# Performance work log

Hardware: AMD Instinct MI355X
Metric: run time of the kernel (lower is better)

The kernel has to match this reference:

```python
import jax, jax.numpy as jnp
import numpy as np

D = 64  # max disparity search range (d in the torch module)


def setup_inputs() -> dict:
    key = jax.random.key(0)
    k1, k2 = jax.random.split(key)
    B, C, H, W = 8, 128, 128, 256
    x1 = jax.random.normal(k1, (B, C, H, W), dtype=jnp.float32)
    x2 = jax.random.normal(k2, (B, C, H, W), dtype=jnp.float32)
    return {"x1": x1, "x2": x2}


def _corr_volume(x1, x2, d):
    # result[n, i, h, w] = (1/C) * sum_c x1[n,c,h,w] * x2[n,c,h,w-i], zero where w-i < 0
    n, c, h, w = x2.shape
    slices = []
    for i in range(d + 1):
        # shift x2 right by i columns, zero-padding on the left
        shifted = jnp.pad(x2[:, :, :, : w - i] if i > 0 else x2,
                          ((0, 0), (0, 0), (0, 0), (i, 0)))
        slices.append(jnp.sum(x1 * shifted, axis=1))  # [n, h, w]
    cv = jnp.stack(slices, axis=1)  # [n, d+1, h, w]
    return cv * (1.0 / c)


def reference(x1, x2):
    return _corr_volume(x1, x2, D)
```

## Files before the change

### kernel.cpp

```cpp
#include <hip/hip_runtime.h>
#include <hip/hip_fp16.h>


constexpr int B   = 8;
constexpr int C   = 128;
constexpr int H   = 128;
constexpr int W   = 256;
constexpr int NI  = 65;
constexpr int HW  = H * W;
constexpr int CHW = C * HW;
constexpr int KC2 = 16;
constexpr int X2W = 320;

typedef _Float16 half2v __attribute__((ext_vector_type(2)));

__device__ inline unsigned int pack2(float a, float b) {
    __half2 h = __floats2half2_rn(a, b);
    return __builtin_bit_cast(unsigned int, h);
}

__device__ inline float fdot2f(unsigned int a, unsigned int b, float c) {
#if __has_builtin(__builtin_amdgcn_fdot2)
    return __builtin_amdgcn_fdot2(__builtin_bit_cast(half2v, a),
                                  __builtin_bit_cast(half2v, b), c, false);
#else
    __half2 ha = __builtin_bit_cast(__half2, a);
    __half2 hb = __builtin_bit_cast(__half2, b);
    float2 fa = __half22float2(ha), fb = __half22float2(hb);
    return fmaf(fa.x, fb.x, fmaf(fa.y, fb.y, c));
#endif
}

__global__ __launch_bounds__(512, 4)
void corr_volume_kernel(const float* __restrict__ x1,
                        const float* __restrict__ x2,
                        float* __restrict__ out) {
    const int h   = blockIdx.x;
    const int n   = blockIdx.y;
    const int tid = threadIdx.x;
    const int l   = tid & 63;
    const int q   = tid >> 6;

    __shared__ unsigned int x1h[KC2][W];
    __shared__ unsigned int x2h[KC2][X2W];

    float acc[8][4];
    #pragma unroll
    for (int il = 0; il < 8; ++il)
        #pragma unroll
        for (int wl = 0; wl < 4; ++wl) acc[il][wl] = 0.0f;
    float acc64[4] = {0.f, 0.f, 0.f, 0.f};

    const int j0 = 4 * l - 8 * q + 56;

    const float* x1g = x1 + n * CHW + h * W;
    const float* x2g = x2 + n * CHW + h * W;

    if (tid < 256) {
        const int r  = tid >> 4;
        const int cq = tid & 15;
        *(uint4*)&x2h[r][4 * cq] = make_uint4(0u, 0u, 0u, 0u);
    }

    for (int c0 = 0; c0 < C; c0 += 2 * KC2) {
        #pragma unroll
        for (int k = 0; k < 2; ++k) {
            const int e  = tid + k * 512;
            const int r  = e >> 6;
            const int cq = e & 63;
            {
                const float4 lo = *(const float4*)(x1g + (c0 + 2 * r) * HW + 4 * cq);
                const float4 hi = *(const float4*)(x1g + (c0 + 2 * r + 1) * HW + 4 * cq);
                uint4 p;
                p.x = pack2(lo.x, hi.x); p.y = pack2(lo.y, hi.y);
                p.z = pack2(lo.z, hi.z); p.w = pack2(lo.w, hi.w);
                *(uint4*)&x1h[r][4 * cq] = p;
            }
            {
                const float4 lo = *(const float4*)(x2g + (c0 + 2 * r) * HW + 4 * cq);
                const float4 hi = *(const float4*)(x2g + (c0 + 2 * r + 1) * HW + 4 * cq);
                uint4 p;
                p.x = pack2(lo.x, hi.x); p.y = pack2(lo.y, hi.y);
                p.z = pack2(lo.z, hi.z); p.w = pack2(lo.w, hi.w);
                *(uint4*)&x2h[r][64 + 4 * cq] = p;
            }
        }
        __syncthreads();

        #pragma unroll 2
        for (int c2 = 0; c2 < KC2; ++c2) {
            const uint4 a4 = *(const uint4*)&x1h[c2][4 * l];
            const unsigned int aw[4] = {a4.x, a4.y, a4.z, a4.w};
            const uint4 b0 = *(const uint4*)&x2h[c2][j0];
            const uint4 b1 = *(const uint4*)&x2h[c2][j0 + 4];
            const uint4 b2 = *(const uint4*)&x2h[c2][j0 + 8];
            const unsigned int bw[12] = {b0.x, b0.y, b0.z, b0.w,
                                         b1.x, b1.y, b1.z, b1.w,
                                         b2.x, b2.y, b2.z, b2.w};
            #pragma unroll
            for (int il = 0; il < 8; ++il)
                #pragma unroll
                for (int wl = 0; wl < 4; ++wl)
                    acc[il][wl] = fdot2f(aw[wl], bw[wl - il + 8], acc[il][wl]);

            if (q == 0) {
                const uint4 d = *(const uint4*)&x2h[c2][4 * l];
                const unsigned int dw[4] = {d.x, d.y, d.z, d.w};
                #pragma unroll
                for (int wl = 0; wl < 4; ++wl)
                    acc64[wl] = fdot2f(aw[wl], dw[wl], acc64[wl]);
            }
        }
        __syncthreads();
    }

    const float scale = 1.0f / (float)C;
    float* outg = out + n * (NI * HW) + h * W + 4 * l;
    #pragma unroll
    for (int il = 0; il < 8; ++il) {
        const int i = 8 * q + il;
        *(float4*)(outg + i * HW) =
            make_float4(acc[il][0] * scale, acc[il][1] * scale,
                        acc[il][2] * scale, acc[il][3] * scale);
    }
    if (q == 0) {
        *(float4*)(outg + 64 * HW) =
            make_float4(acc64[0] * scale, acc64[1] * scale,
                        acc64[2] * scale, acc64[3] * scale);
    }
}

extern "C" void kernel_launch(void* const* d_in, const int* in_sizes, int n_in,
                              void* d_out, int out_size, void* d_ws, size_t ws_size,
                              hipStream_t stream) {
    const float* x1 = (const float*)d_in[0];
    const float* x2 = (const float*)d_in[1];
    float* out = (float*)d_out;
    dim3 grid(H, B);
    corr_volume_kernel<<<grid, 512, 0, stream>>>(x1, x2, out);
}
```

Baseline: 320.0 us.

## Double-buffer shared memory and prefetch next channel chunk into registers

Splits the x1/x2 shared tiles into two buffers. The next chunk's global loads are issued into registers before computing on the current buffer, then packed and stored into the other buffer afterwards, which removes one barrier per iteration. The aim is to hide global load latency behind the fdot2 compute. In exchange it doubles LDS use to about 72KB per block and holds 32 extra VGPRs for the prefetched float4s, which may lower occupancy under launch_bounds(512,4).

```diff
diff --git a/kernel.cpp b/kernel.cpp
--- a/kernel.cpp
+++ b/kernel.cpp
@@ -11,6 +11,7 @@
 constexpr int CHW = C * HW;
 constexpr int KC2 = 16;
 constexpr int X2W = 320;
+constexpr int NCHUNK = C / (2 * KC2);
 
 typedef _Float16 half2v __attribute__((ext_vector_type(2)));
 
@@ -41,8 +42,8 @@
     const int l   = tid & 63;
     const int q   = tid >> 6;
 
-    __shared__ unsigned int x1h[KC2][W];
-    __shared__ unsigned int x2h[KC2][X2W];
+    __shared__ unsigned int x1h[2][KC2][W];
+    __shared__ unsigned int x2h[2][KC2][X2W];
 
     float acc[8][4];
     #pragma unroll
@@ -56,44 +57,66 @@
     const float* x1g = x1 + n * CHW + h * W;
     const float* x2g = x2 + n * CHW + h * W;
 
-    if (tid < 256) {
-        const int r  = tid >> 4;
-        const int cq = tid & 15;
-        *(uint4*)&x2h[r][4 * cq] = make_uint4(0u, 0u, 0u, 0u);
+    {
+        const int bufi = tid >> 8;
+        const int r    = (tid >> 4) & 15;
+        const int cq   = tid & 15;
+        *(uint4*)&x2h[bufi][r][4 * cq] = make_uint4(0u, 0u, 0u, 0u);
     }
 
-    for (int c0 = 0; c0 < C; c0 += 2 * KC2) {
+    const int sr = tid >> 6;
+    const int sc = (tid & 63) * 4;
+
+    float4 L[8];
+
+    auto issue = [&](int c0) {
         #pragma unroll
-        for (int k = 0; k < 2; ++k) {
-            const int e  = tid + k * 512;
-            const int r  = e >> 6;
-            const int cq = e & 63;
-            {
-                const float4 lo = *(const float4*)(x1g + (c0 + 2 * r) * HW + 4 * cq);
-                const float4 hi = *(const float4*)(x1g + (c0 + 2 * r + 1) * HW + 4 * cq);
-                uint4 p;
-                p.x = pack2(lo.x, hi.x); p.y = pack2(lo.y, hi.y);
-                p.z = pack2(lo.z, hi.z); p.w = pack2(lo.w, hi.w);
-                *(uint4*)&x1h[r][4 * cq] = p;
-            }
-            {
-                const float4 lo = *(const float4*)(x2g + (c0 + 2 * r) * HW + 4 * cq);
-                const float4 hi = *(const float4*)(x2g + (c0 + 2 * r + 1) * HW + 4 * cq);
-                uint4 p;
-                p.x = pack2(lo.x, hi.x); p.y = pack2(lo.y, hi.y);
-                p.z = pack2(lo.z, hi.z); p.w = pack2(lo.w, hi.w);
-                *(uint4*)&x2h[r][64 + 4 * cq] = p;
-            }
+        for (int hh = 0; hh < 2; ++hh) {
+            const int r = sr + 8 * hh;
+            const float* a = x1g + (c0 + 2 * r) * HW + sc;
+            const float* b = x2g + (c0 + 2 * r) * HW + sc;
+            L[4 * hh + 0] = *(const float4*)(a);
+            L[4 * hh + 1] = *(const float4*)(a + HW);
+            L[4 * hh + 2] = *(const float4*)(b);
+            L[4 * hh + 3] = *(const float4*)(b + HW);
         }
-        __syncthreads();
+    };
+    auto commit = [&](int bufi) {
+        #pragma unroll
+        for (int hh = 0; hh < 2; ++hh) {
+            const int r = sr + 8 * hh;
+            uint4 p;
+            p.x = pack2(L[4 * hh + 0].x, L[4 * hh + 1].x);
+            p.y = pack2(L[4 * hh + 0].y, L[4 * hh + 1].y);
+            p.z = pack2(L[4 * hh + 0].z, L[4 * hh + 1].z);
+            p.w = pack2(L[4 * hh + 0].w, L[4 * hh + 1].w);
+            *(uint4*)&x1h[bufi][r][sc] = p;
+            uint4 s;
+            s.x = pack2(L[4 * hh + 2].x, L[4 * hh + 3].x);
+            s.y = pack2(L[4 * hh + 2].y, L[4 * hh + 3].y);
+            s.z = pack2(L[4 * hh + 2].z, L[4 * hh + 3].z);
+            s.w = pack2(L[4 * hh + 2].w, L[4 * hh + 3].w);
+            *(uint4*)&x2h[bufi][r][64 + sc] = s;
+        }
+    };
+
+    issue(0);
+    commit(0);
+    __syncthreads();
+
+    #pragma unroll
+    for (int t = 0; t < NCHUNK; ++t) {
+        const int cur = t & 1;
+
+        if (t + 1 < NCHUNK) issue((t + 1) * 2 * KC2);
 
         #pragma unroll 2
         for (int c2 = 0; c2 < KC2; ++c2) {
-            const uint4 a4 = *(const uint4*)&x1h[c2][4 * l];
+            const uint4 a4 = *(const uint4*)&x1h[cur][c2][4 * l];
             const unsigned int aw[4] = {a4.x, a4.y, a4.z, a4.w};
-            const uint4 b0 = *(const uint4*)&x2h[c2][j0];
-            const uint4 b1 = *(const uint4*)&x2h[c2][j0 + 4];
-            const uint4 b2 = *(const uint4*)&x2h[c2][j0 + 8];
+            const uint4 b0 = *(const uint4*)&x2h[cur][c2][j0];
+            const uint4 b1 = *(const uint4*)&x2h[cur][c2][j0 + 4];
+            const uint4 b2 = *(const uint4*)&x2h[cur][c2][j0 + 8];
             const unsigned int bw[12] = {b0.x, b0.y, b0.z, b0.w,
                                          b1.x, b1.y, b1.z, b1.w,
                                          b2.x, b2.y, b2.z, b2.w};
@@ -104,14 +127,18 @@
                     acc[il][wl] = fdot2f(aw[wl], bw[wl - il + 8], acc[il][wl]);
 
             if (q == 0) {
-                const uint4 d = *(const uint4*)&x2h[c2][4 * l];
+                const uint4 d = *(const uint4*)&x2h[cur][c2][4 * l];
                 const unsigned int dw[4] = {d.x, d.y, d.z, d.w};
                 #pragma unroll
                 for (int wl = 0; wl < 4; ++wl)
                     acc64[wl] = fdot2f(aw[wl], dw[wl], acc64[wl]);
             }
         }
-        __syncthreads();
+
+        if (t + 1 < NCHUNK) {
+            commit((t + 1) & 1);
+            __syncthreads();
+        }
     }
 
     const float scale = 1.0f / (float)C;
```

Result: no change. 314.3 us (-1.8%).

## Process two rows per block with 16 disparities per thread

Applied to the files above, without the earlier changes.

Each block now handles two image rows, with four waves per row, and each thread accumulates 16 disparities instead of 8. This raises register reuse of the loaded x2 window, since 20 words are loaded for 64 dot products, and halves the grid. The channel chunk is halved, the trailing barrier is dropped in favour of a leading one, and the disparity-64 term reuses already-loaded registers. The cost is higher register pressure from 64+ accumulators and fewer blocks, which may reduce occupancy.

```diff
diff --git a/kernel.cpp b/kernel.cpp
--- a/kernel.cpp
+++ b/kernel.cpp
@@ -9,8 +9,9 @@
 constexpr int NI  = 65;
 constexpr int HW  = H * W;
 constexpr int CHW = C * HW;
-constexpr int KC2 = 16;
+constexpr int KC2 = 8;
 constexpr int X2W = 320;
+constexpr int NCHUNK = C / (2 * KC2);
 
 typedef _Float16 half2v __attribute__((ext_vector_type(2)));
 
@@ -35,95 +36,100 @@
 void corr_volume_kernel(const float* __restrict__ x1,
                         const float* __restrict__ x2,
                         float* __restrict__ out) {
-    const int h   = blockIdx.x;
+    const int bh  = blockIdx.x;
     const int n   = blockIdx.y;
     const int tid = threadIdx.x;
     const int l   = tid & 63;
     const int q   = tid >> 6;
+    const int hsel = q >> 2;
+    const int qi   = q & 3;
 
-    __shared__ unsigned int x1h[KC2][W];
-    __shared__ unsigned int x2h[KC2][X2W];
+    __shared__ unsigned int x1h[2][KC2][W];
+    __shared__ unsigned int x2h[2][KC2][X2W];
 
-    float acc[8][4];
+    float acc[16][4];
     #pragma unroll
-    for (int il = 0; il < 8; ++il)
+    for (int il = 0; il < 16; ++il)
         #pragma unroll
         for (int wl = 0; wl < 4; ++wl) acc[il][wl] = 0.0f;
     float acc64[4] = {0.f, 0.f, 0.f, 0.f};
 
-    const int j0 = 4 * l - 8 * q + 56;
+    const int j0a = 4 * l - 16 * qi + 48;
 
-    const float* x1g = x1 + n * CHW + h * W;
-    const float* x2g = x2 + n * CHW + h * W;
+    const float* x1b = x1 + n * CHW + (2 * bh) * W;
+    const float* x2b = x2 + n * CHW + (2 * bh) * W;
 
     if (tid < 256) {
-        const int r  = tid >> 4;
+        const int hh = tid >> 7;
+        const int r  = (tid >> 4) & 7;
         const int cq = tid & 15;
-        *(uint4*)&x2h[r][4 * cq] = make_uint4(0u, 0u, 0u, 0u);
+        *(uint4*)&x2h[hh][r][4 * cq] = make_uint4(0u, 0u, 0u, 0u);
     }
 
-    for (int c0 = 0; c0 < C; c0 += 2 * KC2) {
-        #pragma unroll
-        for (int k = 0; k < 2; ++k) {
-            const int e  = tid + k * 512;
-            const int r  = e >> 6;
-            const int cq = e & 63;
-            {
-                const float4 lo = *(const float4*)(x1g + (c0 + 2 * r) * HW + 4 * cq);
-                const float4 hi = *(const float4*)(x1g + (c0 + 2 * r + 1) * HW + 4 * cq);
-                uint4 p;
-                p.x = pack2(lo.x, hi.x); p.y = pack2(lo.y, hi.y);
-                p.z = pack2(lo.z, hi.z); p.w = pack2(lo.w, hi.w);
-                *(uint4*)&x1h[r][4 * cq] = p;
-            }
-            {
-                const float4 lo = *(const float4*)(x2g + (c0 + 2 * r) * HW + 4 * cq);
-                const float4 hi = *(const float4*)(x2g + (c0 + 2 * r + 1) * HW + 4 * cq);
-                uint4 p;
-                p.x = pack2(lo.x, hi.x); p.y = pack2(lo.y, hi.y);
-                p.z = pack2(lo.z, hi.z); p.w = pack2(lo.w, hi.w);
-                *(uint4*)&x2h[r][64 + 4 * cq] = p;
+    for (int t = 0; t < NCHUNK; ++t) {
+        const int c0 = t * 2 * KC2;
+
+        if (t) __syncthreads();
+
+        {
+            const int r = q;
+            #pragma unroll
+            for (int in2 = 0; in2 < 2; ++in2) {
+                const float* gb = in2 ? x2b : x1b;
+                #pragma unroll
+                for (int hh = 0; hh < 2; ++hh) {
+                    const float* g = gb + hh * W + (c0 + 2 * r) * HW + 4 * l;
+                    const float4 lo = *(const float4*)g;
+                    const float4 hi = *(const float4*)(g + HW);
+                    uint4 p;
+                    p.x = pack2(lo.x, hi.x); p.y = pack2(lo.y, hi.y);
+                    p.z = pack2(lo.z, hi.z); p.w = pack2(lo.w, hi.w);
+                    if (in2) *(uint4*)&x2h[hh][r][64 + 4 * l] = p;
+                    else     *(uint4*)&x1h[hh][r][4 * l]      = p;
+                }
             }
         }
         __syncthreads();
 
-        #pragma unroll 2
+        #pragma unroll 1
         for (int c2 = 0; c2 < KC2; ++c2) {
-            const uint4 a4 = *(const uint4*)&x1h[c2][4 * l];
+            const uint4 a4 = *(const uint4*)&x1h[hsel][c2][4 * l];
             const unsigned int aw[4] = {a4.x, a4.y, a4.z, a4.w};
-            const uint4 b0 = *(const uint4*)&x2h[c2][j0];
-            const uint4 b1 = *(const uint4*)&x2h[c2][j0 + 4];
-            const uint4 b2 = *(const uint4*)&x2h[c2][j0 + 8];
-            const unsigned int bw[12] = {b0.x, b0.y, b0.z, b0.w,
+            const uint4 b0 = *(const uint4*)&x2h[hsel][c2][j0a];
+            const uint4 b1 = *(const uint4*)&x2h[hsel][c2][j0a + 4];
+            const uint4 b2 = *(const uint4*)&x2h[hsel][c2][j0a + 8];
+            const uint4 b3 = *(const uint4*)&x2h[hsel][c2][j0a + 12];
+            const uint4 b4 = *(const uint4*)&x2h[hsel][c2][j0a + 16];
+            const unsigned int bw[20] = {b0.x, b0.y, b0.z, b0.w,
                                          b1.x, b1.y, b1.z, b1.w,
-                                         b2.x, b2.y, b2.z, b2.w};
+                                         b2.x, b2.y, b2.z, b2.w,
+                                         b3.x, b3.y, b3.z, b3.w,
+                                         b4.x, b4.y, b4.z, b4.w};
             #pragma unroll
-            for (int il = 0; il < 8; ++il)
+            for (int il = 0; il < 16; ++il)
                 #pragma unroll
                 for (int wl = 0; wl < 4; ++wl)
-                    acc[il][wl] = fdot2f(aw[wl], bw[wl - il + 8], acc[il][wl]);
+                    acc[il][wl] = fdot2f(aw[wl], bw[16 + wl - il], acc[il][wl]);
 
-            if (q == 0) {
-                const uint4 d = *(const uint4*)&x2h[c2][4 * l];
-                const unsigned int dw[4] = {d.x, d.y, d.z, d.w};
+            if (qi == 3) {
                 #pragma unroll
                 for (int wl = 0; wl < 4; ++wl)
-                    acc64[wl] = fdot2f(aw[wl], dw[wl], acc64[wl]);
+                    acc64[wl] = fdot2f(aw[wl], bw[wl], acc64[wl]);
             }
         }
-        __syncthreads();
     }
 
     const float scale = 1.0f / (float)C;
+    const int h = 2 * bh + hsel;
     float* outg = out + n * (NI * HW) + h * W + 4 * l;
     #pragma unroll
-    for (int il = 0; il < 8; ++il) {
-        const int i = 8 * q + il;
+    for (int il = 0; il < 16; ++il) {
+        const int i = 16 * qi + il;
         *(float4*)(outg + i * HW) =
             make_float4(acc[il][0] * scale, acc[il][1] * scale,
                         acc[il][2] * scale, acc[il][3] * scale);
     }
-    if (q == 0) {
+    if (qi == 3) {
         *(float4*)(outg + 64 * HW) =
             make_float4(acc64[0] * scale, acc64[1] * scale,
                         acc64[2] * scale, acc64[3] * scale);
@@ -136,6 +142,6 @@
     const float* x1 = (const float*)d_in[0];
     const float* x2 = (const float*)d_in[1];
     float* out = (float*)d_out;
-    dim3 grid(H, B);
+    dim3 grid(H / 2, B);
     corr_volume_kernel<<<grid, 512, 0, stream>>>(x1, x2, out);
 }
```

New measurement: 308.3 us. 3.7% less time.

## Use fp32 FMAs with double-buffered direct global-to-LDS async loads

Applied to the files above, without the earlier changes.

Drops the fp16 packing and fdot2 path and keeps everything in fp32 with plain FMAs. Input rows are now copied straight into LDS with global_load_lds, skipping the register round-trip and the conversion work. The LDS buffers are double-buffered so the next channel chunk loads while the current one is computed, which should hide load latency and needs only one barrier per chunk. In exchange, LDS use roughly doubles per element and per buffer, which may lower occupancy, and each chunk now does twice as many FMA instructions as the packed fdot2 version.

```diff
diff --git a/kernel.cpp b/kernel.cpp
--- a/kernel.cpp
+++ b/kernel.cpp
@@ -1,5 +1,4 @@
 #include <hip/hip_runtime.h>
-#include <hip/hip_fp16.h>
 
 
 constexpr int B   = 8;
@@ -9,27 +8,9 @@
 constexpr int NI  = 65;
 constexpr int HW  = H * W;
 constexpr int CHW = C * HW;
-constexpr int KC2 = 16;
+constexpr int KC  = 16;
 constexpr int X2W = 320;
-
-typedef _Float16 half2v __attribute__((ext_vector_type(2)));
-
-__device__ inline unsigned int pack2(float a, float b) {
-    __half2 h = __floats2half2_rn(a, b);
-    return __builtin_bit_cast(unsigned int, h);
-}
-
-__device__ inline float fdot2f(unsigned int a, unsigned int b, float c) {
-#if __has_builtin(__builtin_amdgcn_fdot2)
-    return __builtin_amdgcn_fdot2(__builtin_bit_cast(half2v, a),
-                                  __builtin_bit_cast(half2v, b), c, false);
-#else
-    __half2 ha = __builtin_bit_cast(__half2, a);
-    __half2 hb = __builtin_bit_cast(__half2, b);
-    float2 fa = __half22float2(ha), fb = __half22float2(hb);
-    return fmaf(fa.x, fb.x, fmaf(fa.y, fb.y, c));
-#endif
-}
+constexpr int NCHUNK = C / KC;
 
 __global__ __launch_bounds__(512, 4)
 void corr_volume_kernel(const float* __restrict__ x1,
@@ -41,8 +22,8 @@
     const int l   = tid & 63;
     const int q   = tid >> 6;
 
-    __shared__ unsigned int x1h[KC2][W];
-    __shared__ unsigned int x2h[KC2][X2W];
+    __shared__ float x1h[2][KC][W];
+    __shared__ float x2h[2][KC][X2W];
 
     float acc[8][4];
     #pragma unroll
@@ -51,66 +32,69 @@
         for (int wl = 0; wl < 4; ++wl) acc[il][wl] = 0.0f;
     float acc64[4] = {0.f, 0.f, 0.f, 0.f};
 
-    const int j0 = 4 * l - 8 * q + 56;
+    const int j0m8 = 4 * l - 8 * q + 56;
 
     const float* x1g = x1 + n * CHW + h * W;
     const float* x2g = x2 + n * CHW + h * W;
 
-    if (tid < 256) {
-        const int r  = tid >> 4;
-        const int cq = tid & 15;
-        *(uint4*)&x2h[r][4 * cq] = make_uint4(0u, 0u, 0u, 0u);
+    {
+        const int bufi = tid >> 8;
+        const int rr   = (tid >> 4) & 15;
+        const int cq   = tid & 15;
+        *(float4*)&x2h[bufi][rr][4 * cq] = make_float4(0.f, 0.f, 0.f, 0.f);
     }
 
-    for (int c0 = 0; c0 < C; c0 += 2 * KC2) {
+    auto stage = [&](int t, int bufi) {
+        const int c0 = t * KC;
         #pragma unroll
-        for (int k = 0; k < 2; ++k) {
-            const int e  = tid + k * 512;
-            const int r  = e >> 6;
-            const int cq = e & 63;
-            {
-                const float4 lo = *(const float4*)(x1g + (c0 + 2 * r) * HW + 4 * cq);
-                const float4 hi = *(const float4*)(x1g + (c0 + 2 * r + 1) * HW + 4 * cq);
-                uint4 p;
-                p.x = pack2(lo.x, hi.x); p.y = pack2(lo.y, hi.y);
-                p.z = pack2(lo.z, hi.z); p.w = pack2(lo.w, hi.w);
-                *(uint4*)&x1h[r][4 * cq] = p;
-            }
-            {
-                const float4 lo = *(const float4*)(x2g + (c0 + 2 * r) * HW + 4 * cq);
-                const float4 hi = *(const float4*)(x2g + (c0 + 2 * r + 1) * HW + 4 * cq);
-                uint4 p;
-                p.x = pack2(lo.x, hi.x); p.y = pack2(lo.y, hi.y);
-                p.z = pack2(lo.z, hi.z); p.w = pack2(lo.w, hi.w);
-                *(uint4*)&x2h[r][64 + 4 * cq] = p;
-            }
+        for (int rr = 0; rr < 2; ++rr) {
+            const int r = q + 8 * rr;
+            const float* g1 = x1g + (c0 + r) * HW + 4 * l;
+            const float* g2 = x2g + (c0 + r) * HW + 4 * l;
+            __builtin_amdgcn_global_load_lds(
+                (const __attribute__((address_space(1))) void*)g1,
+                (__attribute__((address_space(3))) void*)&x1h[bufi][r][0],
+                16, 0, 0);
+            __builtin_amdgcn_global_load_lds(
+                (const __attribute__((address_space(1))) void*)g2,
+                (__attribute__((address_space(3))) void*)&x2h[bufi][r][64],
+                16, 0, 0);
         }
-        __syncthreads();
+    };
 
-        #pragma unroll 2
-        for (int c2 = 0; c2 < KC2; ++c2) {
-            const uint4 a4 = *(const uint4*)&x1h[c2][4 * l];
-            const unsigned int aw[4] = {a4.x, a4.y, a4.z, a4.w};
-            const uint4 b0 = *(const uint4*)&x2h[c2][j0];
-            const uint4 b1 = *(const uint4*)&x2h[c2][j0 + 4];
-            const uint4 b2 = *(const uint4*)&x2h[c2][j0 + 8];
-            const unsigned int bw[12] = {b0.x, b0.y, b0.z, b0.w,
-                                         b1.x, b1.y, b1.z, b1.w,
-                                         b2.x, b2.y, b2.z, b2.w};
+    stage(0, 0);
+    __syncthreads();
+
+    for (int t = 0; t < NCHUNK; ++t) {
+        const int cur = t & 1;
+
+        if (t + 1 < NCHUNK) stage(t + 1, cur ^ 1);
+
+        #pragma unroll 4
+        for (int c = 0; c < KC; ++c) {
+            const float4 a4 = *(const float4*)&x1h[cur][c][4 * l];
+            const float aw[4] = {a4.x, a4.y, a4.z, a4.w};
+            const float4 b0 = *(const float4*)&x2h[cur][c][j0m8];
+            const float4 b1 = *(const float4*)&x2h[cur][c][j0m8 + 4];
+            const float4 b2 = *(const float4*)&x2h[cur][c][j0m8 + 8];
+            const float bw[12] = {b0.x, b0.y, b0.z, b0.w,
+                                  b1.x, b1.y, b1.z, b1.w,
+                                  b2.x, b2.y, b2.z, b2.w};
             #pragma unroll
             for (int il = 0; il < 8; ++il)
                 #pragma unroll
                 for (int wl = 0; wl < 4; ++wl)
-                    acc[il][wl] = fdot2f(aw[wl], bw[wl - il + 8], acc[il][wl]);
+                    acc[il][wl] = fmaf(aw[wl], bw[8 + wl - il], acc[il][wl]);
 
             if (q == 0) {
-                const uint4 d = *(const uint4*)&x2h[c2][4 * l];
-                const unsigned int dw[4] = {d.x, d.y, d.z, d.w};
+                const float4 d = *(const float4*)&x2h[cur][c][4 * l];
+                const float dw[4] = {d.x, d.y, d.z, d.w};
                 #pragma unroll
                 for (int wl = 0; wl < 4; ++wl)
-                    acc64[wl] = fdot2f(aw[wl], dw[wl], acc64[wl]);
+                    acc64[wl] = fmaf(aw[wl], dw[wl], acc64[wl]);
             }
         }
+
         __syncthreads();
     }
 
```

Result: no change. 322.3 us (+0.7%).
